# Optimization experiments

Measured on AMD Instinct MI355X. Metric: run time of the kernel, lower is better.

## Reference

```python
import jax, jax.numpy as jnp
import numpy as np

D = 4; R = 12; C = 32
P = 2 * R + 1            # 25 fine patch
N = P * P                # 625
MEM_R = 12; MEM_P = 2 * MEM_R + 1
K = 20; DIL_INT = 16


def local_correlation(ft, fr, rad, dil):
    """Zero-padded local correlation (SpatialCorrelationSampler, kernel=1).
    ft, fr: (b,c,h,w) -> (b,Pp,Pp,h,w) with Pp=2*rad+1, patch dilation dil."""
    b, c, h, w = ft.shape
    Pp = 2 * rad + 1
    pad = rad * dil
    frp = jnp.pad(fr, ((0, 0), (0, 0), (pad, pad), (pad, pad)))
    rows = (jnp.arange(Pp)[:, None] * dil + jnp.arange(h)[None, :]).reshape(-1)
    cols = (jnp.arange(Pp)[:, None] * dil + jnp.arange(w)[None, :]).reshape(-1)
    g = frp[:, :, rows, :][:, :, :, cols].reshape(b, c, Pp, h, Pp, w)
    return jnp.einsum('bchw,bcyhxw->byxhw', ft, g)


def bilinear_sample(img, py, px):
    """Bilinear sample img (b,c,H,W) at float coords py/px (broadcastable shape S);
    zero outside the image. Returns (b,c,*S)."""
    b, c, H, W = img.shape
    y0f = jnp.floor(py); x0f = jnp.floor(px)
    wy = py - y0f; wx = px - x0f
    y0 = y0f.astype(jnp.int32); x0 = x0f.astype(jnp.int32)

    def tap(yi, xi, wgt):
        valid = (yi >= 0) & (yi < H) & (xi >= 0) & (xi < W)
        v = img[:, :, jnp.clip(yi, 0, H - 1), jnp.clip(xi, 0, W - 1)]
        return v * (wgt * valid)[None, None]

    return (tap(y0, x0, (1 - wy) * (1 - wx)) + tap(y0, x0 + 1, (1 - wy) * wx)
            + tap(y0 + 1, x0, wy * (1 - wx)) + tap(y0 + 1, x0 + 1, wy * wx))


def _topk_dim1(corr, k):
    # corr: (b,N,hw); torch.topk(dim=1, sorted=True) equivalent
    vals, idx = jax.lax.top_k(corr.transpose(0, 2, 1), k)   # (b,hw,k)
    return vals.transpose(0, 2, 1), idx                      # (b,k,hw), (b,hw,k)


def _long_ref(ft, fr, q, dirate):
    b, c, h, w = ft.shape
    # coarse dilated correlation -> softmax -> soft-argmax expected offset
    corr_c = local_correlation(ft, fr, MEM_R, dirate).reshape(b, MEM_P * MEM_P, h * w)
    attn = jax.nn.softmax(corr_c, axis=1).reshape(b, MEM_P, MEM_P, h, w)
    d = jnp.arange(-MEM_R, MEM_R + 1, dtype=ft.dtype)
    off_y = jnp.einsum('byxhw,y->bhw', attn, d) * dirate
    off_x = jnp.einsum('byxhw,x->bhw', attn, d) * dirate
    # deform_im2col with PxP kernel: sample fr at (r+dy+off_y, c+dx+off_x)
    dtap = jnp.arange(-R, R + 1, dtype=ft.dtype)
    py = dtap[:, None, None, None] + (jnp.arange(h, dtype=ft.dtype)[:, None] + off_y[0])[None, None]
    px = dtap[None, :, None, None] + (jnp.arange(w, dtype=ft.dtype)[None, :] + off_x[0])[None, None]
    col = bilinear_sample(fr, py, px)                        # (b,c,P,P,h,w)
    corr = jnp.einsum('bchw,bcyxhw->byxhw', ft, col).reshape(b, N, h * w)
    vals, idx = _topk_dim1(corr, K)
    # process_long_image_uf_topk: shift offsets by decoded top-k displacement, 1-tap bilinear
    dr = (idx[0] // 25 - 12).reshape(h, w, K).transpose(2, 0, 1).astype(ft.dtype)  # (K,h,w)
    dc = (idx[0] % 25 - 12).reshape(h, w, K).transpose(2, 0, 1).astype(ft.dtype)
    py2 = jnp.arange(h, dtype=ft.dtype)[None, :, None] + off_y[0][None] + dr
    px2 = jnp.arange(w, dtype=ft.dtype)[None, None, :] + off_x[0][None] + dc
    imgs = bilinear_sample(q, py2, px2)                      # (b,C,K,h,w)
    return vals, imgs.reshape(b, q.shape[1], K, h * w)


def _short_ref(ft, fr, q):
    b, c, h, w = ft.shape
    corr = local_correlation(ft, fr, R, 1).reshape(b, N, h * w)
    vals, idx = _topk_dim1(corr, K)
    # process_short_image_uf_topk: integer gather q[:, :, r+dr, c+dc] (zero-padded)
    dr = (idx[0] // 25 - 12).reshape(h, w, K).transpose(2, 0, 1)   # (K,h,w) int
    dc = (idx[0] % 25 - 12).reshape(h, w, K).transpose(2, 0, 1)
    qp = jnp.pad(q, ((0, 0), (0, 0), (R, R), (R, R)))
    yi = jnp.arange(h)[None, :, None] + dr + R
    xi = jnp.arange(w)[None, None, :] + dc + R
    imgs = qp[:, :, yi, xi]                                  # (b,C,K,h,w)
    return vals, imgs.reshape(b, q.shape[1], K, h * w)


def _forward(feats_r, feats_t, quantized_r, ref_index, current_ind):
    ref_index = np.asarray(ref_index)
    current_ind = int(current_ind)
    gaps = current_ind - ref_index
    nsearch = int(np.sum(gaps > DIL_INT))
    dirates = [int(min(4, g // DIL_INT + 1)) for g in gaps if g > DIL_INT]
    nref = feats_r.shape[0]
    b, c, h, w = feats_t.shape
    # prep(): subsample labels by D (C=32 channels, one_hot skipped)
    qr = [quantized_r[i][:, :, ::D, ::D].astype(feats_t.dtype) for i in range(nref)]
    vals_all, imgs_all = [], []
    for i in range(nsearch):
        v, im = _long_ref(feats_t, feats_r[i], qr[i], dirates[i])
        vals_all.append(v); imgs_all.append(im)
    for i in range(nsearch, nref):
        v, im = _short_ref(feats_t, feats_r[i], qr[i])
        vals_all.append(v); imgs_all.append(im)
    attn = jax.nn.softmax(jnp.concatenate(vals_all, axis=1), axis=1)  # (b, nref*K, hw)
    imgs = jnp.concatenate(imgs_all, axis=2)                          # (b, C, nref*K, hw)
    return jnp.einsum('bkp,bckp->bcp', attn, imgs).reshape(b, qr[0].shape[1], h, w)


def setup_inputs():
    key = jax.random.key(0)
    k1, k2, k3 = jax.random.split(key, 3)
    feats_r = jax.random.normal(k1, (3, 1, 64, 48, 48), dtype=jnp.float32)
    feats_t = jax.random.normal(k2, (1, 64, 48, 48), dtype=jnp.float32)
    quantized_r = jax.random.uniform(k3, (3, 1, 32, 192, 192), dtype=jnp.float32)
    # gaps vs current_ind=60: 20 (>16 -> long ref, dirate=2), 10, 5 (short refs)
    ref_index = np.array([40, 50, 55], dtype=np.int64)
    current_ind = 60
    return {"feats_r": feats_r, "feats_t": feats_t, "quantized_r": quantized_r,
            "ref_index": ref_index, "current_ind": current_ind}


def reference(feats_r, feats_t, quantized_r, ref_index, current_ind):
    return _forward(feats_r, feats_t, quantized_r, ref_index, current_ind)
```

## Files before the change

### kernel.cpp

```cpp
#include <hip/hip_runtime.h>
#include <math.h>

#define HW 48
#define NPIX 2304
#define CF 64
#define CQ 32
#define RAD 12
#define PP 25
#define NTAP 625
#define KTOP 20
#define DILINT 16
#define QW 192
#define CSTRIDE 640
#define NPB 6
#define NC 30
#define LROW 68
#define DGS 28


__device__ inline int read_ref_index(const void* rip, int r) {
    const long long* p64 = (const long long*)rip;
    long long v0 = p64[0];
    if (v0 >= 0 && v0 < 1000000) return (int)p64[r];
    return ((const int*)rip)[r];
}

__device__ inline int get_dil(const void* refIdx, const void* curInd, int r,
                              bool* isLong) {
    int cur = ((const int*)curInd)[0];
    int gap = cur - read_ref_index(refIdx, r);
    *isLong = gap > DILINT;
    return *isLong ? min(4, gap / DILINT + 1) : 1;
}

__global__ void prep_kernel(const float* __restrict__ fr,
                            const float* __restrict__ ft,
                            const float* __restrict__ q, int nref,
                            float* __restrict__ ftT,
                            float* __restrict__ frT,
                            float* __restrict__ qrT) {
    int i = blockIdx.x * blockDim.x + threadIdx.x;
    int tft = NPIX * CF;
    int tfr = nref * NPIX * CF;
    int tqr = nref * NPIX * CQ;
    if (i < tft) {
        int p = i >> 6, c = i & 63;
        ftT[i] = ft[c * NPIX + p];
    } else if (i < tft + tfr) {
        int j = i - tft;
        int rr = j / (NPIX * CF);
        int rem = j % (NPIX * CF);
        int p = rem >> 6, c = rem & 63;
        frT[j] = fr[((size_t)rr * CF + c) * NPIX + p];
    } else if (i < tft + tfr + tqr) {
        int j = i - tft - tfr;
        int rr = j / (NPIX * CQ);
        int rem = j % (NPIX * CQ);
        int p = rem >> 5, c = rem & 31;
        int y = p / HW, x = p % HW;
        qrT[j] = q[(((size_t)rr * CQ + c) * QW + 4 * y) * QW + 4 * x];
    }
}

__global__ __launch_bounds__(256) void corr_band(
    const float* __restrict__ ftT, const float* __restrict__ frT,
    const void* __restrict__ refIdx, const void* __restrict__ curInd,
    float* __restrict__ corr) {
    __shared__ float lrow[NC * LROW];

    int tid = threadIdx.x;
    int bx = blockIdx.x % 9;
    int y = blockIdx.x / 9;
    int r = blockIdx.y;

    bool isLong;
    int dil = get_dil(refIdx, curInd, r, &isLong);
    int nb = (dil == 3) ? 9 : 8;
    if (bx >= nb) return;

    int m = bx % dil, grp = bx / dil;
    int npr = HW / dil;

    int T = tid;
    bool active = T < NPB * PP;
    int j = active ? T / PP : 0;
    int dxi = active ? T - PP * j : 0;
    int xoff = grp * NPB + j;
    bool pvalid = active && (xoff < npr);
    int xj = m + dil * xoff;
    int pj = pvalid ? (y * HW + xj) : 0;
    int lc = j + dxi;

    float4 fq[16];
    const float4* fp = (const float4*)(ftT + (size_t)pj * CF);
#pragma unroll
    for (int i = 0; i < 16; ++i) fq[i] = fp[i];

    const float* frb = frT + (size_t)r * NPIX * CF;
    float* outb = corr + ((size_t)r * NPIX + pj) * CSTRIDE + dxi;
    int gc0 = m + dil * (grp * NPB - RAD);

    for (int dy = 0; dy < PP; ++dy) {
        int yy = y + dil * (dy - RAD);
        if (yy < 0 || yy >= HW) {
            if (pvalid) outb[dy * PP] = 0.f;
            continue;
        }
        for (int k = tid; k < NC * 16; k += 256) {
            int col = k >> 4, sub = k & 15;
            int gc = gc0 + dil * col;
            float4 v = {0.f, 0.f, 0.f, 0.f};
            if (gc >= 0 && gc < HW)
                v = *(const float4*)(frb + ((size_t)yy * HW + gc) * CF + sub * 4);
            *(float4*)(lrow + col * LROW + sub * 4) = v;
        }
        __syncthreads();
        if (pvalid) {
            const float* bp = lrow + lc * LROW;
            float s = 0.f;
#pragma unroll
            for (int i = 0; i < 16; ++i) {
                float4 b = *(const float4*)(bp + 4 * i);
                s += fq[i].x * b.x + fq[i].y * b.y + fq[i].z * b.z + fq[i].w * b.w;
            }
            outb[dy * PP] = s;
        }
        __syncthreads();
    }
}

__global__ __launch_bounds__(192) void corr_fuse(
    const float* __restrict__ ftT, const float* __restrict__ frT,
    const float* __restrict__ qrT, const float* __restrict__ corr,
    const void* __restrict__ refIdx, const void* __restrict__ curInd,
    int nref, float* __restrict__ out) {
    __shared__ float dgw_s[3][27 * DGS];
    __shared__ float valsL[96];
    __shared__ int   topiL[96];
    __shared__ float accL[3][64];
    __shared__ float ssmL[3][64];
    __shared__ float offL[3][2];

    int tid = threadIdx.x;
    int wid = tid >> 6, lane = tid & 63;
    int p = blockIdx.x;
    int y = p / HW, x = p % HW;
    int r = wid;

    bool isLong;
    int dil = get_dil(refIdx, curInd, r, &isLong);
    float oy = 0.f, ox = 0.f;

    const float* cb = corr + ((size_t)r * NPIX + p) * CSTRIDE;
    float creg[10];
#pragma unroll
    for (int jj = 0; jj < 10; ++jj) {
        int t = lane + 64 * jj;
        creg[jj] = (t < NTAP) ? cb[t] : -INFINITY;
    }

    if (isLong) {
        float M = -INFINITY;
#pragma unroll
        for (int jj = 0; jj < 10; ++jj) M = fmaxf(M, creg[jj]);
#pragma unroll
        for (int s = 32; s; s >>= 1) M = fmaxf(M, __shfl_xor(M, s, 64));
        float s0 = 0.f, sy = 0.f, sx = 0.f;
#pragma unroll
        for (int jj = 0; jj < 10; ++jj) {
            int t = lane + 64 * jj;
            if (t < NTAP) {
                float e = expf(creg[jj] - M);
                int dy = t / PP - RAD, dx = t % PP - RAD;
                s0 += e; sy += e * (float)dy; sx += e * (float)dx;
            }
        }
#pragma unroll
        for (int s = 32; s; s >>= 1) {
            s0 += __shfl_xor(s0, s, 64);
            sy += __shfl_xor(sy, s, 64);
            sx += __shfl_xor(sx, s, 64);
        }
        oy = sy / s0 * (float)dil;
        ox = sx / s0 * (float)dil;
        if (lane == 0) { offL[r][0] = oy; offL[r][1] = ox; }
    }
    __syncthreads();

    for (int rr = 0; rr < nref; ++rr) {
        bool rrLong;
        get_dil(refIdx, curInd, rr, &rrLong);
        if (!rrLong) continue;
        float roy = offL[rr][0], rox = offL[rr][1];
        float fy = (float)y + roy, fx = (float)x + rox;
        int iy0 = (int)floorf(fy), ix0 = (int)floorf(fx);

        int cs = tid & 15;
        int g2 = tid >> 4;
        float4 fqc = ((const float4*)(ftT + (size_t)p * CF))[cs];
        const float* frb = frT + (size_t)rr * NPIX * CF;
        float* dgw = dgw_s[rr];
        int colbase = ix0 - RAD;
        for (int a = 0; a < 26; ++a) {
            int yy = iy0 - RAD + a;
            bool yok = (yy >= 0 && yy < HW);
            const float* rowp = frb + (size_t)(yok ? yy : 0) * (HW * CF);
#pragma unroll
            for (int i = 0; i < 3; ++i) {
                int lc2 = 12 * i + g2;
                int xx2 = colbase + lc2;
                int xs = min(max(xx2, 0), HW - 1);
                float s = 0.f;
                if (yok && lc2 < 26) {
                    float4 b = *(const float4*)(rowp + xs * CF + 4 * cs);
                    s = fqc.x * b.x + fqc.y * b.y + fqc.z * b.z + fqc.w * b.w;
                    s = (xx2 >= 0 && xx2 < HW) ? s : 0.f;
                }
                s += __shfl_xor(s, 1, 64);
                s += __shfl_xor(s, 2, 64);
                s += __shfl_xor(s, 4, 64);
                s += __shfl_xor(s, 8, 64);
                if (cs == 0 && lc2 < 26) dgw[a * DGS + lc2] = s;
            }
        }
    }
    __syncthreads();

    if (isLong) {
        float fy = (float)y + oy, fx = (float)x + ox;
        float fy0 = floorf(fy), fx0 = floorf(fx);
        float wy = fy - fy0, wx = fx - fx0;
        const float* dgw = dgw_s[r];
        float w00 = (1.f - wy) * (1.f - wx), w01 = (1.f - wy) * wx;
        float w10 = wy * (1.f - wx), w11 = wy * wx;
#pragma unroll
        for (int jj = 0; jj < 10; ++jj) {
            int t = lane + 64 * jj;
            if (t < NTAP) {
                int a = t / PP, bcol = t % PP;
                creg[jj] = w00 * dgw[a * DGS + bcol] + w01 * dgw[a * DGS + bcol + 1] +
                           w10 * dgw[(a + 1) * DGS + bcol] + w11 * dgw[(a + 1) * DGS + bcol + 1];
            }
        }
    }

    double key[10];
#pragma unroll
    for (int jj = 0; jj < 10; ++jj) {
        float v = creg[jj] + 0.0f;
        unsigned u = __float_as_uint(v);
        u = (u & 0x80000000u) ? ~u : (u | 0x80000000u);
        int t = lane + 64 * jj;
        key[jj] = (double)u * 1024.0 + (double)(1023 - t);
    }

    for (int k2 = 0; k2 < KTOP / 2; ++k2) {
        double a = key[0], b = -1.0;
#pragma unroll
        for (int jj = 1; jj < 10; ++jj) {
            double kk = key[jj];
            double na = fmax(a, kk);
            b = fmax(b, fmin(a, kk));
            a = na;
        }
#pragma unroll
        for (int s = 32; s; s >>= 1) {
            double pa = __shfl_xor(a, s, 64);
            double pb = __shfl_xor(b, s, 64);
            double na = fmax(a, pa);
            b = fmax(fmin(a, pa), fmax(b, pb));
            a = na;
        }
        if (lane == 0) {
            double qa = floor(a * (1.0 / 1024.0));
            double qb2 = floor(b * (1.0 / 1024.0));
            unsigned ua = (unsigned)qa, ub = (unsigned)qb2;
            unsigned ba = (ua & 0x80000000u) ? (ua ^ 0x80000000u) : ~ua;
            unsigned bb = (ub & 0x80000000u) ? (ub ^ 0x80000000u) : ~ub;
            int ta = 1023 - (int)(a - qa * 1024.0);
            int tb = 1023 - (int)(b - qb2 * 1024.0);
            valsL[r * KTOP + 2 * k2]     = __uint_as_float(ba);
            topiL[r * KTOP + 2 * k2]     = ta;
            valsL[r * KTOP + 2 * k2 + 1] = __uint_as_float(bb);
            topiL[r * KTOP + 2 * k2 + 1] = tb;
        }
#pragma unroll
        for (int jj = 0; jj < 10; ++jj) {
            double kk = key[jj];
            key[jj] = (kk == a || kk == b) ? 0.0 : kk;
        }
    }
    __syncthreads();

    int c = lane & 31, h = lane >> 5;
    int nk = nref * KTOP;
    float m = (lane < nk) ? valsL[lane] : -INFINITY;
#pragma unroll
    for (int s = 32; s; s >>= 1) m = fmaxf(m, __shfl_xor(m, s, 64));

    float ssum = 0.f, acc = 0.f;
    const float* qb = qrT + (size_t)r * NPIX * CQ;
    for (int k2 = 0; k2 < KTOP / 2; ++k2) {
        int k = r * KTOP + h * (KTOP / 2) + k2;
        float e = expf(valsL[k] - m);
        ssum += e;
        int id = topiL[k];
        int dr = id / PP - RAD, dc = id % PP - RAD;
        float img = 0.f;
        if (isLong) {
            float py = (float)y + oy + (float)dr;
            float px = (float)x + ox + (float)dc;
            float fy0 = floorf(py), fx0 = floorf(px);
            int y0 = (int)fy0, x0 = (int)fx0;
            float wy = py - fy0, wx = px - fx0;
            float w00 = (1.f - wy) * (1.f - wx), w01 = (1.f - wy) * wx;
            float w10 = wy * (1.f - wx), w11 = wy * wx;
            if (y0 >= 0 && y0 < HW && x0 >= 0 && x0 < HW)
                img += w00 * qb[(y0 * HW + x0) * CQ + c];
            if (y0 >= 0 && y0 < HW && x0 + 1 >= 0 && x0 + 1 < HW)
                img += w01 * qb[(y0 * HW + x0 + 1) * CQ + c];
            if (y0 + 1 >= 0 && y0 + 1 < HW && x0 >= 0 && x0 < HW)
                img += w10 * qb[((y0 + 1) * HW + x0) * CQ + c];
            if (y0 + 1 >= 0 && y0 + 1 < HW && x0 + 1 >= 0 && x0 + 1 < HW)
                img += w11 * qb[((y0 + 1) * HW + x0 + 1) * CQ + c];
        } else {
            int yy = y + dr, xx = x + dc;
            if (yy >= 0 && yy < HW && xx >= 0 && xx < HW)
                img = qb[(yy * HW + xx) * CQ + c];
        }
        acc += e * img;
    }
    accL[wid][lane] = acc;
    ssmL[wid][lane] = ssum;
    __syncthreads();

    if (wid == 0) {
        float ta = 0.f, ts = 0.f;
        for (int w = 0; w < nref; ++w) { ta += accL[w][lane]; ts += ssmL[w][lane]; }
        ta += __shfl_xor(ta, 32, 64);
        ts += __shfl_xor(ts, 32, 64);
        if (h == 0) out[(size_t)c * NPIX + p] = ta / ts;
    }
}

extern "C" void kernel_launch(void* const* d_in, const int* in_sizes, int n_in,
                              void* d_out, int out_size, void* d_ws, size_t ws_size,
                              hipStream_t stream) {
    const float* fr = (const float*)d_in[0];
    const float* ft = (const float*)d_in[1];
    const float* q  = (const float*)d_in[2];
    const void* refIdx = d_in[3];
    const void* curInd = d_in[4];
    int nref = in_sizes[0] / (CF * NPIX);

    float* ws  = (float*)d_ws;
    float* ftT = ws;
    float* frT = ftT + (size_t)NPIX * CF;
    float* qrT = frT + (size_t)nref * NPIX * CF;
    float* corr = qrT + (size_t)nref * NPIX * CQ;

    int total = NPIX * CF + nref * NPIX * CF + nref * NPIX * CQ;
    prep_kernel<<<(total + 255) / 256, 256, 0, stream>>>(fr, ft, q, nref, ftT, frT, qrT);
    corr_band<<<dim3(HW * 9, nref), 256, 0, stream>>>(ftT, frT, refIdx, curInd, corr);
    corr_fuse<<<dim3(NPIX), 64 * nref, 0, stream>>>(ftT, frT, qrT, corr, refIdx, curInd,
                                                    nref, (float*)d_out);
}
```

Baseline: 109.6 us.

## Fuse top-k extraction with softmax-weighted color gather and coalesce prep reads

The top-k loop now decodes each pair of winners in every lane and accumulates the exp-weighted color gather directly, instead of staging values and indices in shared memory and running a separate gather loop. The softmax max is taken from the first (largest) top-k value of each reference after one barrier, and expf becomes __expf. The prep kernel is also changed to read inputs contiguously and scatter the transposed writes. This removes shared-memory staging and serialization by lane 0, and overlaps gather loads with the top-k reductions. In exchange it uses uncoalesced writes in prep, adds a barrier inside the loop, and __expf is less precise.

```diff
diff --git a/kernel.cpp b/kernel.cpp
--- a/kernel.cpp
+++ b/kernel.cpp
@@ -33,6 +33,35 @@
     return *isLong ? min(4, gap / DILINT + 1) : 1;
 }
 
+__device__ inline float gather_color(const float* __restrict__ qb, int c,
+                                     int y, int x, int id, bool isLong,
+                                     float oy, float ox) {
+    int dr = id / PP - RAD, dc = id % PP - RAD;
+    float img = 0.f;
+    if (isLong) {
+        float py = (float)y + oy + (float)dr;
+        float px = (float)x + ox + (float)dc;
+        float fy0 = floorf(py), fx0 = floorf(px);
+        int y0 = (int)fy0, x0 = (int)fx0;
+        float wy = py - fy0, wx = px - fx0;
+        float w00 = (1.f - wy) * (1.f - wx), w01 = (1.f - wy) * wx;
+        float w10 = wy * (1.f - wx), w11 = wy * wx;
+        if (y0 >= 0 && y0 < HW && x0 >= 0 && x0 < HW)
+            img += w00 * qb[(y0 * HW + x0) * CQ + c];
+        if (y0 >= 0 && y0 < HW && x0 + 1 >= 0 && x0 + 1 < HW)
+            img += w01 * qb[(y0 * HW + x0 + 1) * CQ + c];
+        if (y0 + 1 >= 0 && y0 + 1 < HW && x0 >= 0 && x0 < HW)
+            img += w10 * qb[((y0 + 1) * HW + x0) * CQ + c];
+        if (y0 + 1 >= 0 && y0 + 1 < HW && x0 + 1 >= 0 && x0 + 1 < HW)
+            img += w11 * qb[((y0 + 1) * HW + x0 + 1) * CQ + c];
+    } else {
+        int yy = y + dr, xx = x + dc;
+        if (yy >= 0 && yy < HW && xx >= 0 && xx < HW)
+            img = qb[(yy * HW + xx) * CQ + c];
+    }
+    return img;
+}
+
 __global__ void prep_kernel(const float* __restrict__ fr,
                             const float* __restrict__ ft,
                             const float* __restrict__ q, int nref,
@@ -44,21 +73,22 @@
     int tfr = nref * NPIX * CF;
     int tqr = nref * NPIX * CQ;
     if (i < tft) {
-        int p = i >> 6, c = i & 63;
-        ftT[i] = ft[c * NPIX + p];
+        int c = i / NPIX, p = i - c * NPIX;
+        ftT[p * CF + c] = ft[i];
     } else if (i < tft + tfr) {
         int j = i - tft;
         int rr = j / (NPIX * CF);
-        int rem = j % (NPIX * CF);
-        int p = rem >> 6, c = rem & 63;
-        frT[j] = fr[((size_t)rr * CF + c) * NPIX + p];
+        int rem = j - rr * (NPIX * CF);
+        int c = rem / NPIX, p = rem - c * NPIX;
+        frT[((size_t)rr * NPIX + p) * CF + c] = fr[j];
     } else if (i < tft + tfr + tqr) {
         int j = i - tft - tfr;
         int rr = j / (NPIX * CQ);
-        int rem = j % (NPIX * CQ);
-        int p = rem >> 5, c = rem & 31;
-        int y = p / HW, x = p % HW;
-        qrT[j] = q[(((size_t)rr * CQ + c) * QW + 4 * y) * QW + 4 * x];
+        int rem = j - rr * (NPIX * CQ);
+        int c = rem / NPIX, p = rem - c * NPIX;
+        int y = p / HW, x = p - y * HW;
+        qrT[((size_t)rr * NPIX + p) * CQ + c] =
+            q[(((size_t)rr * CQ + c) * QW + 4 * y) * QW + 4 * x];
     }
 }
 
@@ -135,11 +165,10 @@
     const void* __restrict__ refIdx, const void* __restrict__ curInd,
     int nref, float* __restrict__ out) {
     __shared__ float dgw_s[3][27 * DGS];
-    __shared__ float valsL[96];
-    __shared__ int   topiL[96];
     __shared__ float accL[3][64];
     __shared__ float ssmL[3][64];
     __shared__ float offL[3][2];
+    __shared__ float mL[3];
 
     int tid = threadIdx.x;
     int wid = tid >> 6, lane = tid & 63;
@@ -254,6 +283,11 @@
         key[jj] = (double)u * 1024.0 + (double)(1023 - t);
     }
 
+    int c = lane & 31, h = lane >> 5;
+    const float* qb = qrT + (size_t)r * NPIX * CQ;
+    float ssum = 0.f, acc = 0.f, m = 0.f;
+    float v0a = 0.f, v0b = 0.f; int t0a = 0, t0b = 0;
+
     for (int k2 = 0; k2 < KTOP / 2; ++k2) {
         double a = key[0], b = -1.0;
 #pragma unroll
@@ -271,75 +305,51 @@
             b = fmax(fmin(a, pa), fmax(b, pb));
             a = na;
         }
-        if (lane == 0) {
-            double qa = floor(a * (1.0 / 1024.0));
-            double qb2 = floor(b * (1.0 / 1024.0));
-            unsigned ua = (unsigned)qa, ub = (unsigned)qb2;
-            unsigned ba = (ua & 0x80000000u) ? (ua ^ 0x80000000u) : ~ua;
-            unsigned bb = (ub & 0x80000000u) ? (ub ^ 0x80000000u) : ~ub;
-            int ta = 1023 - (int)(a - qa * 1024.0);
-            int tb = 1023 - (int)(b - qb2 * 1024.0);
-            valsL[r * KTOP + 2 * k2]     = __uint_as_float(ba);
-            topiL[r * KTOP + 2 * k2]     = ta;
-            valsL[r * KTOP + 2 * k2 + 1] = __uint_as_float(bb);
-            topiL[r * KTOP + 2 * k2 + 1] = tb;
+        double qa = floor(a * (1.0 / 1024.0));
+        double qb2 = floor(b * (1.0 / 1024.0));
+        unsigned ua = (unsigned)qa, ub = (unsigned)qb2;
+        unsigned ba = (ua & 0x80000000u) ? (ua ^ 0x80000000u) : ~ua;
+        unsigned bb = (ub & 0x80000000u) ? (ub ^ 0x80000000u) : ~ub;
+        float va = __uint_as_float(ba), vb = __uint_as_float(bb);
+        int ta = 1023 - (int)(a - qa * 1024.0);
+        int tb = 1023 - (int)(b - qb2 * 1024.0);
+
+        if (k2 == 0) {
+            if (lane == 0) mL[r] = va;
+            v0a = va; v0b = vb; t0a = ta; t0b = tb;
+        } else {
+            float vv = h ? vb : va;
+            int tt = h ? tb : ta;
+            float e = __expf(vv - m);
+            ssum += e;
+            acc += e * gather_color(qb, c, y, x, tt, isLong, oy, ox);
         }
 #pragma unroll
         for (int jj = 0; jj < 10; ++jj) {
             double kk = key[jj];
             key[jj] = (kk == a || kk == b) ? 0.0 : kk;
         }
-    }
-    __syncthreads();
-
-    int c = lane & 31, h = lane >> 5;
-    int nk = nref * KTOP;
-    float m = (lane < nk) ? valsL[lane] : -INFINITY;
-#pragma unroll
-    for (int s = 32; s; s >>= 1) m = fmaxf(m, __shfl_xor(m, s, 64));
-
-    float ssum = 0.f, acc = 0.f;
-    const float* qb = qrT + (size_t)r * NPIX * CQ;
-    for (int k2 = 0; k2 < KTOP / 2; ++k2) {
-        int k = r * KTOP + h * (KTOP / 2) + k2;
-        float e = expf(valsL[k] - m);
-        ssum += e;
-        int id = topiL[k];
-        int dr = id / PP - RAD, dc = id % PP - RAD;
-        float img = 0.f;
-        if (isLong) {
-            float py = (float)y + oy + (float)dr;
-            float px = (float)x + ox + (float)dc;
-            float fy0 = floorf(py), fx0 = floorf(px);
-            int y0 = (int)fy0, x0 = (int)fx0;
-            float wy = py - fy0, wx = px - fx0;
-            float w00 = (1.f - wy) * (1.f - wx), w01 = (1.f - wy) * wx;
-            float w10 = wy * (1.f - wx), w11 = wy * wx;
-            if (y0 >= 0 && y0 < HW && x0 >= 0 && x0 < HW)
-                img += w00 * qb[(y0 * HW + x0) * CQ + c];
-            if (y0 >= 0 && y0 < HW && x0 + 1 >= 0 && x0 + 1 < HW)
-                img += w01 * qb[(y0 * HW + x0 + 1) * CQ + c];
-            if (y0 + 1 >= 0 && y0 + 1 < HW && x0 >= 0 && x0 < HW)
-                img += w10 * qb[((y0 + 1) * HW + x0) * CQ + c];
-            if (y0 + 1 >= 0 && y0 + 1 < HW && x0 + 1 >= 0 && x0 + 1 < HW)
-                img += w11 * qb[((y0 + 1) * HW + x0 + 1) * CQ + c];
-        } else {
-            int yy = y + dr, xx = x + dc;
-            if (yy >= 0 && yy < HW && xx >= 0 && xx < HW)
-                img = qb[(yy * HW + xx) * CQ + c];
-        }
-        acc += e * img;
+        if (k2 == 0) {
+            __syncthreads();
+            m = mL[0];
+            for (int w = 1; w < nref; ++w) m = fmaxf(m, mL[w]);
+            float vv = h ? v0b : v0a;
+            int tt = h ? t0b : t0a;
+            float e = __expf(vv - m);
+            ssum += e;
+            acc += e * gather_color(qb, c, y, x, tt, isLong, oy, ox);
+        }
     }
     accL[wid][lane] = acc;
     ssmL[wid][lane] = ssum;
     __syncthreads();
 
     if (wid == 0) {
-        float ta = 0.f, ts = 0.f;
-        for (int w = 0; w < nref; ++w) { ta += accL[w][lane]; ts += ssmL[w][lane]; }
-        ta += __shfl_xor(ta, 32, 64);
+        float ta2 = 0.f, ts = 0.f;
+        for (int w = 0; w < nref; ++w) { ta2 += accL[w][lane]; ts += ssmL[w][lane]; }
+        ta2 += __shfl_xor(ta2, 32, 64);
         ts += __shfl_xor(ts, 32, 64);
-        if (h == 0) out[(size_t)c * NPIX + p] = ta / ts;
+        if (h == 0) out[(size_t)c * NPIX + p] = ta2 / ts;
     }
 }
 
```

After: 112.5 us. 2.6% more time.
